# Kernel optimization log

Measured on AMD Instinct MI355X. Metric: run time of the kernel, lower is better.

The kernel has to match this reference:

```python
import jax, jax.numpy as jnp
import numpy as np

B, T, D, U, O = 256, 512, 256, 512, 64  # batch, n_steps, feature_in, units, n_output


def setup_inputs() -> dict:
    key = jax.random.key(0)
    k_x, k_wx, k_wh, k_wd = jax.random.split(key, 4)
    x = jax.random.normal(k_x, (B, T, D), dtype=jnp.float32)
    # Lecun-normal-ish init scales so activations stay sane
    Wx = jax.random.normal(k_wx, (D, 4 * U), dtype=jnp.float32) * (1.0 / np.sqrt(D))
    Wh = jax.random.normal(k_wh, (U, 4 * U), dtype=jnp.float32) * (1.0 / np.sqrt(U))
    b = jnp.zeros((4 * U,), dtype=jnp.float32)
    Wd = jax.random.normal(k_wd, (U, O), dtype=jnp.float32) * (1.0 / np.sqrt(U))
    bd = jnp.zeros((O,), dtype=jnp.float32)
    return {"x": x, "Wx": Wx, "Wh": Wh, "b": b, "Wd": Wd, "bd": bd}


def reference(x, Wx, Wh, b, Wd, bd):
    """Sequential LSTM scan (flax nn.LSTMCell math) + per-step dense decode.

    x: [B, T, D] -> y: [B, T, O]
    """
    batch = x.shape[0]
    units = Wh.shape[0]
    c0 = jnp.zeros((batch, units), dtype=x.dtype)
    h0 = jnp.zeros((batch, units), dtype=x.dtype)

    def step(carry, xt):
        c, h = carry
        gates = xt @ Wx + h @ Wh + b            # [B, 4U]
        i, f, g, o = jnp.split(gates, 4, axis=-1)
        i = jax.nn.sigmoid(i)
        f = jax.nn.sigmoid(f)
        g = jnp.tanh(g)
        o = jax.nn.sigmoid(o)
        c_new = f * c + i * g
        h_new = o * jnp.tanh(c_new)
        y = h_new @ Wd + bd                     # [B, O]
        return (c_new, h_new), y

    xs = jnp.swapaxes(x, 0, 1)                  # [T, B, D]
    _, ys = jax.lax.scan(step, (c0, h0), xs)    # ys: [T, B, O]
    return jnp.swapaxes(ys, 0, 1)               # [B, T, O]
```

## Files before the change

### kernel.cpp

```cpp
#include <hip/hip_runtime.h>


#define Bb 256
#define Tt 512
#define Dd 256
#define Uu 512
#define Oo 64

typedef short bs8 __attribute__((ext_vector_type(8)));
typedef float f32x4 __attribute__((ext_vector_type(4)));

__device__ __forceinline__ unsigned short f2bf(float f) {
  unsigned u = __float_as_uint(f);
  u += 0x7fffu + ((u >> 16) & 1u);
  return (unsigned short)(u >> 16);
}
__device__ __forceinline__ float bf2f(unsigned short s) {
  return __uint_as_float(((unsigned)s) << 16);
}
__device__ __forceinline__ float sigm(float v) { return 1.0f / (1.0f + __expf(-v)); }
__device__ __forceinline__ float tanhfast(float v) { return 2.0f / (1.0f + __expf(-2.0f * v)) - 1.0f; }

__device__ __forceinline__ int zbyte(int row, int k) {
  return (row * 1536 + k * 2) ^ ((row & 7) << 4);
}

__global__ void rnn_init_bar(unsigned* bar) {
  for (int i = threadIdx.x; i < 16 * 32 * 32; i += 256)
    __hip_atomic_store(&bar[i], 0u, __ATOMIC_RELAXED, __HIP_MEMORY_SCOPE_AGENT);
}

__launch_bounds__(256, 2)
__global__ void rnn_lstm_kernel(const float* __restrict__ x, const float* __restrict__ Wx,
                                const float* __restrict__ Wh, const float* __restrict__ bias,
                                const float* __restrict__ Wd, const float* __restrict__ bd,
                                float* __restrict__ out, unsigned short* hbuf, unsigned* bar) {
  __shared__ __align__(16) char zs[16 * 768 * 2];
  __shared__ float gates[4][16][17];
  __shared__ float wdl[512][2];
  __shared__ float ypart[16][2][16];

  const int tid = threadIdx.x;
  const int lane = tid & 63;
  const int wid = tid >> 6;
  const int bid = blockIdx.x;
  const int bg = (bid & 7) | ((bid >> 8) << 3);
  const int ug = (bid >> 3) & 31;
  const int b_base = bg * 16;
  const int u_base = ug * 16;
  const int oc0 = ug * 2;

  unsigned* fl = bar + bg * 32 * 32;

  bs8 breg[24];
  {
    const int gc = wid * 512 + u_base + (lane & 15);
    const int kfr = (lane >> 4) * 8;
#pragma unroll
    for (int ks = 0; ks < 24; ++ks) {
      bs8 bb;
#pragma unroll
      for (int e = 0; e < 8; ++e) {
        int kg = ks * 32 + kfr + e;
        float w = (kg < 256) ? Wx[(size_t)kg * 2048 + gc]
                             : Wh[(size_t)(kg - 256) * 2048 + gc];
        bb[e] = (short)f2bf(w);
      }
      breg[ks] = bb;
    }
  }

  const int prow = tid & 15;
  const int usec = tid >> 4;
  const int us4 = usec & 3;
  float bi[4], bff[4], bgg[4], boo[4];
  if (tid < 64) {
#pragma unroll
    for (int j = 0; j < 4; ++j) {
      int ugl = u_base + us4 * 4 + j;
      bi[j]  = bias[0 * 512 + ugl];
      bff[j] = bias[1 * 512 + ugl];
      bgg[j] = bias[2 * 512 + ugl];
      boo[j] = bias[3 * 512 + ugl];
    }
  }
  float cst[4] = {0.f, 0.f, 0.f, 0.f};

  union U16 { unsigned long long q[2]; bs8 v; };

#pragma unroll
  for (int i = 0; i < 4; ++i) {
    int c = tid + i * 256;
    int u = c >> 1, oc = c & 1;
    wdl[u][oc] = Wd[(size_t)u * Oo + oc0 + oc];
  }
  {
    int row = tid >> 4;
    int d0 = (tid & 15) * 16;
    const float* xp = x + ((size_t)(b_base + row) * Tt + 0) * Dd + d0;
    float4 v0 = *(const float4*)xp;
    float4 v1 = *(const float4*)(xp + 4);
    float4 v2 = *(const float4*)(xp + 8);
    float4 v3 = *(const float4*)(xp + 12);
    bs8 p0, p1;
    p0[0] = (short)f2bf(v0.x); p0[1] = (short)f2bf(v0.y);
    p0[2] = (short)f2bf(v0.z); p0[3] = (short)f2bf(v0.w);
    p0[4] = (short)f2bf(v1.x); p0[5] = (short)f2bf(v1.y);
    p0[6] = (short)f2bf(v1.z); p0[7] = (short)f2bf(v1.w);
    p1[0] = (short)f2bf(v2.x); p1[1] = (short)f2bf(v2.y);
    p1[2] = (short)f2bf(v2.z); p1[3] = (short)f2bf(v2.w);
    p1[4] = (short)f2bf(v3.x); p1[5] = (short)f2bf(v3.y);
    p1[6] = (short)f2bf(v3.z); p1[7] = (short)f2bf(v3.w);
    *(bs8*)(zs + zbyte(row, d0)) = p0;
    *(bs8*)(zs + zbyte(row, d0 + 8)) = p1;
  }
#pragma unroll
  for (int i = 0; i < 4; ++i) {
    int c = tid + i * 256;
    int row = c >> 6;
    int u0 = (c & 63) * 8;
    bs8 zz = {0, 0, 0, 0, 0, 0, 0, 0};
    *(bs8*)(zs + zbyte(row, 256 + u0)) = zz;
  }
  __syncthreads();

  for (int t = 0; t < Tt; ++t) {
    f32x4 acc0 = {0, 0, 0, 0}, acc1 = {0, 0, 0, 0};
    {
      const int arow = lane & 15;
      const int akf = (lane >> 4) * 8;
#pragma unroll
      for (int ks = 0; ks < 24; ks += 2) {
        bs8 av0 = *(const bs8*)(zs + zbyte(arow, ks * 32 + akf));
        bs8 av1 = *(const bs8*)(zs + zbyte(arow, (ks + 1) * 32 + akf));
        acc0 = __builtin_amdgcn_mfma_f32_16x16x32_bf16(av0, breg[ks], acc0, 0, 0, 0);
        acc1 = __builtin_amdgcn_mfma_f32_16x16x32_bf16(av1, breg[ks + 1], acc1, 0, 0, 0);
      }
      acc0 += acc1;
    }
    {
      const int u16 = lane & 15;
      const int rb = (lane >> 4) * 4;
#pragma unroll
      for (int j = 0; j < 4; ++j) gates[wid][rb + j][u16] = acc0[j];
    }
    __syncthreads();

    if (tid < 64) {
      unsigned long long hpack = 0ull;
#pragma unroll
      for (int j = 0; j < 4; ++j) {
        int u = us4 * 4 + j;
        float gi = gates[0][prow][u] + bi[j];
        float gf = gates[1][prow][u] + bff[j];
        float gg = gates[2][prow][u] + bgg[j];
        float go = gates[3][prow][u] + boo[j];
        float iv = sigm(gi), fv = sigm(gf), gv = tanhfast(gg), ov = sigm(go);
        float cn = fv * cst[j] + iv * gv;
        cst[j] = cn;
        float hv = ov * tanhfast(cn);
        hpack |= ((unsigned long long)f2bf(hv)) << (16 * j);
      }
      unsigned long long* hp =
          (unsigned long long*)(hbuf + (size_t)(t & 1) * Bb * Uu +
                                (size_t)(b_base + prow) * Uu + u_base + us4 * 4);
      unsigned long long old = __hip_atomic_exchange(hp, hpack, __ATOMIC_RELAXED,
                                                     __HIP_MEMORY_SCOPE_AGENT);
      asm volatile("" :: "v"(old));
    }
    __syncthreads();
    if (tid == 0) {
      unsigned oldf = __hip_atomic_exchange(&fl[ug * 32], (unsigned)(t + 1),
                                            __ATOMIC_RELAXED, __HIP_MEMORY_SCOPE_AGENT);
      asm volatile("" :: "v"(oldf));
    }

    if (t + 1 < Tt) {
      int row = tid >> 4;
      int d0 = (tid & 15) * 16;
      const float* xp = x + ((size_t)(b_base + row) * Tt + (t + 1)) * Dd + d0;
      float4 v0 = *(const float4*)xp;
      float4 v1 = *(const float4*)(xp + 4);
      float4 v2 = *(const float4*)(xp + 8);
      float4 v3 = *(const float4*)(xp + 12);
      bs8 p0, p1;
      p0[0] = (short)f2bf(v0.x); p0[1] = (short)f2bf(v0.y);
      p0[2] = (short)f2bf(v0.z); p0[3] = (short)f2bf(v0.w);
      p0[4] = (short)f2bf(v1.x); p0[5] = (short)f2bf(v1.y);
      p0[6] = (short)f2bf(v1.z); p0[7] = (short)f2bf(v1.w);
      p1[0] = (short)f2bf(v2.x); p1[1] = (short)f2bf(v2.y);
      p1[2] = (short)f2bf(v2.z); p1[3] = (short)f2bf(v2.w);
      p1[4] = (short)f2bf(v3.x); p1[5] = (short)f2bf(v3.y);
      p1[6] = (short)f2bf(v3.z); p1[7] = (short)f2bf(v3.w);
      *(bs8*)(zs + zbyte(row, d0)) = p0;
      *(bs8*)(zs + zbyte(row, d0 + 8)) = p1;
    }

    if (t > 0) {
      float s0 = 0.f, s1 = 0.f;
#pragma unroll
      for (int c8 = 0; c8 < 4; ++c8) {
        int k = 256 + usec * 32 + c8 * 8;
        bs8 hv = *(const bs8*)(zs + zbyte(prow, k));
#pragma unroll
        for (int e = 0; e < 8; ++e) {
          float hf = bf2f((unsigned short)hv[e]);
          int u = usec * 32 + c8 * 8 + e;
          s0 += hf * wdl[u][0];
          s1 += hf * wdl[u][1];
        }
      }
      ypart[prow][0][usec] = s0;
      ypart[prow][1][usec] = s1;
    }
    __syncthreads();
    if (t > 0 && tid < 32) {
      int b = tid >> 1, oc = tid & 1;
      float s = bd[oc0 + oc];
#pragma unroll
      for (int q = 0; q < 16; ++q) s += ypart[b][oc][q];
      out[((size_t)(b_base + b) * Tt + (t - 1)) * Oo + oc0 + oc] = s;
    }
    if (wid == 1) {
      for (;;) {
        unsigned v = __hip_atomic_load(&fl[(lane & 31) * 32], __ATOMIC_RELAXED,
                                       __HIP_MEMORY_SCOPE_AGENT);
        if (!__any((int)(v < (unsigned)(t + 1)))) break;
        __builtin_amdgcn_s_sleep(2);
      }
    }
    __builtin_amdgcn_sched_barrier(0);
    __syncthreads();

    {
      const unsigned short* hsrc = hbuf + (size_t)(t & 1) * Bb * Uu;
#pragma unroll
      for (int i = 0; i < 4; ++i) {
        int c = tid + i * 256;
        int row = c >> 6;
        int u0 = (c & 63) * 8;
        const unsigned long long* p =
            (const unsigned long long*)(hsrc + (size_t)(b_base + row) * Uu + u0);
        U16 uu;
        uu.q[0] = __hip_atomic_load(p, __ATOMIC_RELAXED, __HIP_MEMORY_SCOPE_AGENT);
        uu.q[1] = __hip_atomic_load(p + 1, __ATOMIC_RELAXED, __HIP_MEMORY_SCOPE_AGENT);
        *(bs8*)(zs + zbyte(row, 256 + u0)) = uu.v;
      }
    }
    __syncthreads();
  }

  {
    float s0 = 0.f, s1 = 0.f;
#pragma unroll
    for (int c8 = 0; c8 < 4; ++c8) {
      int k = 256 + usec * 32 + c8 * 8;
      bs8 hv = *(const bs8*)(zs + zbyte(prow, k));
#pragma unroll
      for (int e = 0; e < 8; ++e) {
        float hf = bf2f((unsigned short)hv[e]);
        int u = usec * 32 + c8 * 8 + e;
        s0 += hf * wdl[u][0];
        s1 += hf * wdl[u][1];
      }
    }
    ypart[prow][0][usec] = s0;
    ypart[prow][1][usec] = s1;
    __syncthreads();
    if (tid < 32) {
      int b = tid >> 1, oc = tid & 1;
      float s = bd[oc0 + oc];
#pragma unroll
      for (int q = 0; q < 16; ++q) s += ypart[b][oc][q];
      out[((size_t)(b_base + b) * Tt + (Tt - 1)) * Oo + oc0 + oc] = s;
    }
  }
}

extern "C" void kernel_launch(void* const* d_in, const int* in_sizes, int n_in,
                              void* d_out, int out_size, void* d_ws, size_t ws_size,
                              hipStream_t stream) {
  const float* x  = (const float*)d_in[0];
  const float* Wx = (const float*)d_in[1];
  const float* Wh = (const float*)d_in[2];
  const float* bs = (const float*)d_in[3];
  const float* Wd = (const float*)d_in[4];
  const float* bd = (const float*)d_in[5];
  float* out = (float*)d_out;

  unsigned short* hbuf = (unsigned short*)d_ws;
  unsigned* bar = (unsigned*)((char*)d_ws + (size_t)2 * Bb * Uu * 2);

  rnn_init_bar<<<1, 256, 0, stream>>>(bar);
  rnn_lstm_kernel<<<dim3(512), dim3(256), 0, stream>>>(x, Wx, Wh, bs, Wd, bd, out, hbuf, bar);
}
```

Measured before the change: 2.424 ms.

## Compute dense decode with MFMA and prefetch next-step x before gate matmul

The per-step output projection h@Wd, previously a scalar FMA loop over LDS-staged Wd with a 16-way partial reduction, now runs on MFMA with Wd held in registers as bf16 fragments (only 2 of 16 columns used). The decode is merged into the gate-matmul phase and its store into the cell-update phase, which removes one __syncthreads per step. The next timestep's x is loaded into registers before the matmul so global latency overlaps compute, and bf16 packing uses paired conversion intrinsics. Wd is now rounded to bf16, which lowers decode precision, and the extra fragment registers add pressure on top of 24 resident weight fragments.

```diff
diff --git a/kernel.cpp b/kernel.cpp
--- a/kernel.cpp
+++ b/kernel.cpp
@@ -1,4 +1,5 @@
 #include <hip/hip_runtime.h>
+#include <hip/hip_bf16.h>
 
 
 #define Bb 256
@@ -15,8 +16,10 @@
   u += 0x7fffu + ((u >> 16) & 1u);
   return (unsigned short)(u >> 16);
 }
-__device__ __forceinline__ float bf2f(unsigned short s) {
-  return __uint_as_float(((unsigned)s) << 16);
+__device__ __forceinline__ unsigned f2bf2(float lo, float hi) {
+  union { __hip_bfloat162 b; unsigned u; } cv;
+  cv.b = __float22bfloat162_rn(make_float2(lo, hi));
+  return cv.u;
 }
 __device__ __forceinline__ float sigm(float v) { return 1.0f / (1.0f + __expf(-v)); }
 __device__ __forceinline__ float tanhfast(float v) { return 2.0f / (1.0f + __expf(-2.0f * v)) - 1.0f; }
@@ -37,8 +40,7 @@
                                 float* __restrict__ out, unsigned short* hbuf, unsigned* bar) {
   __shared__ __align__(16) char zs[16 * 768 * 2];
   __shared__ float gates[4][16][17];
-  __shared__ float wdl[512][2];
-  __shared__ float ypart[16][2][16];
+  __shared__ float yp[4][16][2];
 
   const int tid = threadIdx.x;
   const int lane = tid & 63;
@@ -69,10 +71,25 @@
       breg[ks] = bb;
     }
   }
+  bs8 wdfrag[4];
+  {
+    const int col = lane & 15;
+    const int kfr = (lane >> 4) * 8;
+#pragma unroll
+    for (int i = 0; i < 4; ++i) {
+      int ksl = wid * 4 + i;
+      bs8 bb;
+#pragma unroll
+      for (int e = 0; e < 8; ++e) {
+        int u = ksl * 32 + kfr + e;
+        bb[e] = (col < 2) ? (short)f2bf(Wd[(size_t)u * Oo + oc0 + col]) : (short)0;
+      }
+      wdfrag[i] = bb;
+    }
+  }
 
   const int prow = tid & 15;
-  const int usec = tid >> 4;
-  const int us4 = usec & 3;
+  const int us4 = (tid >> 4) & 3;
   float bi[4], bff[4], bgg[4], boo[4];
   if (tid < 64) {
 #pragma unroll
@@ -88,12 +105,6 @@
 
   union U16 { unsigned long long q[2]; bs8 v; };
 
-#pragma unroll
-  for (int i = 0; i < 4; ++i) {
-    int c = tid + i * 256;
-    int u = c >> 1, oc = c & 1;
-    wdl[u][oc] = Wd[(size_t)u * Oo + oc0 + oc];
-  }
   {
     int row = tid >> 4;
     int d0 = (tid & 15) * 16;
@@ -102,17 +113,13 @@
     float4 v1 = *(const float4*)(xp + 4);
     float4 v2 = *(const float4*)(xp + 8);
     float4 v3 = *(const float4*)(xp + 12);
-    bs8 p0, p1;
-    p0[0] = (short)f2bf(v0.x); p0[1] = (short)f2bf(v0.y);
-    p0[2] = (short)f2bf(v0.z); p0[3] = (short)f2bf(v0.w);
-    p0[4] = (short)f2bf(v1.x); p0[5] = (short)f2bf(v1.y);
-    p0[6] = (short)f2bf(v1.z); p0[7] = (short)f2bf(v1.w);
-    p1[0] = (short)f2bf(v2.x); p1[1] = (short)f2bf(v2.y);
-    p1[2] = (short)f2bf(v2.z); p1[3] = (short)f2bf(v2.w);
-    p1[4] = (short)f2bf(v3.x); p1[5] = (short)f2bf(v3.y);
-    p1[6] = (short)f2bf(v3.z); p1[7] = (short)f2bf(v3.w);
-    *(bs8*)(zs + zbyte(row, d0)) = p0;
-    *(bs8*)(zs + zbyte(row, d0 + 8)) = p1;
+    uint4 p0, p1;
+    p0.x = f2bf2(v0.x, v0.y); p0.y = f2bf2(v0.z, v0.w);
+    p0.z = f2bf2(v1.x, v1.y); p0.w = f2bf2(v1.z, v1.w);
+    p1.x = f2bf2(v2.x, v2.y); p1.y = f2bf2(v2.z, v2.w);
+    p1.z = f2bf2(v3.x, v3.y); p1.w = f2bf2(v3.z, v3.w);
+    *(uint4*)(zs + zbyte(row, d0)) = p0;
+    *(uint4*)(zs + zbyte(row, d0 + 8)) = p1;
   }
 #pragma unroll
   for (int i = 0; i < 4; ++i) {
@@ -124,30 +131,53 @@
   }
   __syncthreads();
 
+  const int arow = lane & 15;
+  const int akf = (lane >> 4) * 8;
+  const int rb = (lane >> 4) * 4;
+
   for (int t = 0; t < Tt; ++t) {
+    float4 xv0, xv1, xv2, xv3;
+    const int xrow = tid >> 4;
+    const int xd0 = (tid & 15) * 16;
+    if (t + 1 < Tt) {
+      const float* xp = x + ((size_t)(b_base + xrow) * Tt + (t + 1)) * Dd + xd0;
+      xv0 = *(const float4*)xp;
+      xv1 = *(const float4*)(xp + 4);
+      xv2 = *(const float4*)(xp + 8);
+      xv3 = *(const float4*)(xp + 12);
+    }
+
     f32x4 acc0 = {0, 0, 0, 0}, acc1 = {0, 0, 0, 0};
+#pragma unroll
+    for (int ks = 0; ks < 24; ks += 2) {
+      bs8 av0 = *(const bs8*)(zs + zbyte(arow, ks * 32 + akf));
+      bs8 av1 = *(const bs8*)(zs + zbyte(arow, (ks + 1) * 32 + akf));
+      acc0 = __builtin_amdgcn_mfma_f32_16x16x32_bf16(av0, breg[ks], acc0, 0, 0, 0);
+      acc1 = __builtin_amdgcn_mfma_f32_16x16x32_bf16(av1, breg[ks + 1], acc1, 0, 0, 0);
+    }
+    acc0 += acc1;
     {
-      const int arow = lane & 15;
-      const int akf = (lane >> 4) * 8;
-#pragma unroll
-      for (int ks = 0; ks < 24; ks += 2) {
-        bs8 av0 = *(const bs8*)(zs + zbyte(arow, ks * 32 + akf));
-        bs8 av1 = *(const bs8*)(zs + zbyte(arow, (ks + 1) * 32 + akf));
-        acc0 = __builtin_amdgcn_mfma_f32_16x16x32_bf16(av0, breg[ks], acc0, 0, 0, 0);
-        acc1 = __builtin_amdgcn_mfma_f32_16x16x32_bf16(av1, breg[ks + 1], acc1, 0, 0, 0);
-      }
-      acc0 += acc1;
+      f32x4 yacc = {0, 0, 0, 0};
+#pragma unroll
+      for (int i = 0; i < 4; ++i) {
+        int ks = 8 + wid * 4 + i;
+        bs8 av = *(const bs8*)(zs + zbyte(arow, ks * 32 + akf));
+        yacc = __builtin_amdgcn_mfma_f32_16x16x32_bf16(av, wdfrag[i], yacc, 0, 0, 0);
+      }
+      if ((lane & 15) < 2) {
+#pragma unroll
+        for (int j = 0; j < 4; ++j) yp[wid][rb + j][lane & 15] = yacc[j];
+      }
     }
     {
       const int u16 = lane & 15;
-      const int rb = (lane >> 4) * 4;
 #pragma unroll
       for (int j = 0; j < 4; ++j) gates[wid][rb + j][u16] = acc0[j];
     }
     __syncthreads();
 
     if (tid < 64) {
-      unsigned long long hpack = 0ull;
+      float hv[4];
 #pragma unroll
       for (int j = 0; j < 4; ++j) {
         int u = us4 * 4 + j;
@@ -158,15 +188,21 @@
         float iv = sigm(gi), fv = sigm(gf), gv = tanhfast(gg), ov = sigm(go);
         float cn = fv * cst[j] + iv * gv;
         cst[j] = cn;
-        float hv = ov * tanhfast(cn);
-        hpack |= ((unsigned long long)f2bf(hv)) << (16 * j);
-      }
+        hv[j] = ov * tanhfast(cn);
+      }
+      unsigned long long hpack =
+          (unsigned long long)f2bf2(hv[0], hv[1]) |
+          ((unsigned long long)f2bf2(hv[2], hv[3]) << 32);
       unsigned long long* hp =
           (unsigned long long*)(hbuf + (size_t)(t & 1) * Bb * Uu +
                                 (size_t)(b_base + prow) * Uu + u_base + us4 * 4);
       unsigned long long old = __hip_atomic_exchange(hp, hpack, __ATOMIC_RELAXED,
                                                      __HIP_MEMORY_SCOPE_AGENT);
       asm volatile("" :: "v"(old));
+    } else if (t > 0 && tid >= 128 && tid < 160) {
+      int b = (tid - 128) >> 1, oc = tid & 1;
+      float s = bd[oc0 + oc] + yp[0][b][oc] + yp[1][b][oc] + yp[2][b][oc] + yp[3][b][oc];
+      out[((size_t)(b_base + b) * Tt + (t - 1)) * Oo + oc0 + oc] = s;
     }
     __syncthreads();
     if (tid == 0) {
@@ -176,50 +212,13 @@
     }
 
     if (t + 1 < Tt) {
-      int row = tid >> 4;
-      int d0 = (tid & 15) * 16;
-      const float* xp = x + ((size_t)(b_base + row) * Tt + (t + 1)) * Dd + d0;
-      float4 v0 = *(const float4*)xp;
-      float4 v1 = *(const float4*)(xp + 4);
-      float4 v2 = *(const float4*)(xp + 8);
-      float4 v3 = *(const float4*)(xp + 12);
-      bs8 p0, p1;
-      p0[0] = (short)f2bf(v0.x); p0[1] = (short)f2bf(v0.y);
-      p0[2] = (short)f2bf(v0.z); p0[3] = (short)f2bf(v0.w);
-      p0[4] = (short)f2bf(v1.x); p0[5] = (short)f2bf(v1.y);
-      p0[6] = (short)f2bf(v1.z); p0[7] = (short)f2bf(v1.w);
-      p1[0] = (short)f2bf(v2.x); p1[1] = (short)f2bf(v2.y);
-      p1[2] = (short)f2bf(v2.z); p1[3] = (short)f2bf(v2.w);
-      p1[4] = (short)f2bf(v3.x); p1[5] = (short)f2bf(v3.y);
-      p1[6] = (short)f2bf(v3.z); p1[7] = (short)f2bf(v3.w);
-      *(bs8*)(zs + zbyte(row, d0)) = p0;
-      *(bs8*)(zs + zbyte(row, d0 + 8)) = p1;
-    }
-
-    if (t > 0) {
-      float s0 = 0.f, s1 = 0.f;
-#pragma unroll
-      for (int c8 = 0; c8 < 4; ++c8) {
-        int k = 256 + usec * 32 + c8 * 8;
-        bs8 hv = *(const bs8*)(zs + zbyte(prow, k));
-#pragma unroll
-        for (int e = 0; e < 8; ++e) {
-          float hf = bf2f((unsigned short)hv[e]);
-          int u = usec * 32 + c8 * 8 + e;
-          s0 += hf * wdl[u][0];
-          s1 += hf * wdl[u][1];
-        }
-      }
-      ypart[prow][0][usec] = s0;
-      ypart[prow][1][usec] = s1;
-    }
-    __syncthreads();
-    if (t > 0 && tid < 32) {
-      int b = tid >> 1, oc = tid & 1;
-      float s = bd[oc0 + oc];
-#pragma unroll
-      for (int q = 0; q < 16; ++q) s += ypart[b][oc][q];
-      out[((size_t)(b_base + b) * Tt + (t - 1)) * Oo + oc0 + oc] = s;
+      uint4 p0, p1;
+      p0.x = f2bf2(xv0.x, xv0.y); p0.y = f2bf2(xv0.z, xv0.w);
+      p0.z = f2bf2(xv1.x, xv1.y); p0.w = f2bf2(xv1.z, xv1.w);
+      p1.x = f2bf2(xv2.x, xv2.y); p1.y = f2bf2(xv2.z, xv2.w);
+      p1.z = f2bf2(xv3.x, xv3.y); p1.w = f2bf2(xv3.z, xv3.w);
+      *(uint4*)(zs + zbyte(xrow, xd0)) = p0;
+      *(uint4*)(zs + zbyte(xrow, xd0 + 8)) = p1;
     }
     if (wid == 1) {
       for (;;) {
@@ -251,27 +250,21 @@
   }
 
   {
-    float s0 = 0.f, s1 = 0.f;
-#pragma unroll
-    for (int c8 = 0; c8 < 4; ++c8) {
-      int k = 256 + usec * 32 + c8 * 8;
-      bs8 hv = *(const bs8*)(zs + zbyte(prow, k));
-#pragma unroll
-      for (int e = 0; e < 8; ++e) {
-        float hf = bf2f((unsigned short)hv[e]);
-        int u = usec * 32 + c8 * 8 + e;
-        s0 += hf * wdl[u][0];
-        s1 += hf * wdl[u][1];
-      }
-    }
-    ypart[prow][0][usec] = s0;
-    ypart[prow][1][usec] = s1;
+    f32x4 yacc = {0, 0, 0, 0};
+#pragma unroll
+    for (int i = 0; i < 4; ++i) {
+      int ks = 8 + wid * 4 + i;
+      bs8 av = *(const bs8*)(zs + zbyte(arow, ks * 32 + akf));
+      yacc = __builtin_amdgcn_mfma_f32_16x16x32_bf16(av, wdfrag[i], yacc, 0, 0, 0);
+    }
+    if ((lane & 15) < 2) {
+#pragma unroll
+      for (int j = 0; j < 4; ++j) yp[wid][rb + j][lane & 15] = yacc[j];
+    }
     __syncthreads();
     if (tid < 32) {
       int b = tid >> 1, oc = tid & 1;
-      float s = bd[oc0 + oc];
-#pragma unroll
-      for (int q = 0; q < 16; ++q) s += ypart[b][oc][q];
+      float s = bd[oc0 + oc] + yp[0][b][oc] + yp[1][b][oc] + yp[2][b][oc] + yp[3][b][oc];
       out[((size_t)(b_base + b) * Tt + (Tt - 1)) * Oo + oc0 + oc] = s;
     }
   }
```

Measured after the change: 2.691 ms. 1.11x slower.

## Assign LSTM work by XCD so each batch group's barrier stays within one XCD

Applied to the files above, without the earlier changes.

Each block reads its hardware XCC id and takes a slot from a per-XCD atomic counter. The slot determines its batch group and unit group, so all 32 blocks sharing a batch-group barrier run on the same XCD. Flag publish and polling then switch to workgroup-scope atomics (polling becomes a fetch_add of zero), aiming to keep barrier traffic in the XCD-local L2 instead of going cross-die. Extra dynamic LDS is requested, which changes occupancy. This relies on blocks being spread evenly across XCDs and on weaker-scope atomics still being visible to other CUs, which risks incorrect synchronisation or deadlock.

```diff
diff --git a/kernel.cpp b/kernel.cpp
--- a/kernel.cpp
+++ b/kernel.cpp
@@ -26,7 +26,7 @@
 }
 
 __global__ void rnn_init_bar(unsigned* bar) {
-  for (int i = threadIdx.x; i < 16 * 32 * 32; i += 256)
+  for (int i = threadIdx.x; i < 16 * 32 * 32 + 8 * 32; i += 256)
     __hip_atomic_store(&bar[i], 0u, __ATOMIC_RELAXED, __HIP_MEMORY_SCOPE_AGENT);
 }
 
@@ -39,13 +39,24 @@
   __shared__ float gates[4][16][17];
   __shared__ float wdl[512][2];
   __shared__ float ypart[16][2][16];
+  __shared__ unsigned slotsh;
 
   const int tid = threadIdx.x;
   const int lane = tid & 63;
   const int wid = tid >> 6;
-  const int bid = blockIdx.x;
-  const int bg = (bid & 7) | ((bid >> 8) << 3);
-  const int ug = (bid >> 3) & 31;
+
+  unsigned xcd;
+  asm("s_getreg_b32 %0, hwreg(HW_REG_XCC_ID)" : "=s"(xcd));
+  xcd &= 7u;
+  if (tid == 0) {
+    unsigned* cnts = bar + 16 * 32 * 32;
+    slotsh = __hip_atomic_fetch_add(&cnts[xcd * 32], 1u, __ATOMIC_RELAXED,
+                                    __HIP_MEMORY_SCOPE_AGENT);
+  }
+  __syncthreads();
+  const unsigned s = slotsh & 63u;
+  const int bg = (int)xcd + 8 * (int)(s & 1u);
+  const int ug = (int)(s >> 1) & 31;
   const int b_base = bg * 16;
   const int u_base = ug * 16;
   const int oc0 = ug * 2;
@@ -171,7 +182,7 @@
     __syncthreads();
     if (tid == 0) {
       unsigned oldf = __hip_atomic_exchange(&fl[ug * 32], (unsigned)(t + 1),
-                                            __ATOMIC_RELAXED, __HIP_MEMORY_SCOPE_AGENT);
+                                            __ATOMIC_RELAXED, __HIP_MEMORY_SCOPE_WORKGROUP);
       asm volatile("" :: "v"(oldf));
     }
 
@@ -216,15 +227,17 @@
     __syncthreads();
     if (t > 0 && tid < 32) {
       int b = tid >> 1, oc = tid & 1;
-      float s = bd[oc0 + oc];
-#pragma unroll
-      for (int q = 0; q < 16; ++q) s += ypart[b][oc][q];
-      out[((size_t)(b_base + b) * Tt + (t - 1)) * Oo + oc0 + oc] = s;
+      float s2 = bd[oc0 + oc];
+#pragma unroll
+      for (int q = 0; q < 16; ++q) s2 += ypart[b][oc][q];
+      out[((size_t)(b_base + b) * Tt + (t - 1)) * Oo + oc0 + oc] = s2;
     }
     if (wid == 1) {
+      unsigned zero = 0;
+      asm volatile("" : "+v"(zero));
       for (;;) {
-        unsigned v = __hip_atomic_load(&fl[(lane & 31) * 32], __ATOMIC_RELAXED,
-                                       __HIP_MEMORY_SCOPE_AGENT);
+        unsigned v = __hip_atomic_fetch_add(&fl[(lane & 31) * 32], zero,
+                                            __ATOMIC_RELAXED, __HIP_MEMORY_SCOPE_WORKGROUP);
         if (!__any((int)(v < (unsigned)(t + 1)))) break;
         __builtin_amdgcn_s_sleep(2);
       }
@@ -269,10 +282,10 @@
     __syncthreads();
     if (tid < 32) {
       int b = tid >> 1, oc = tid & 1;
-      float s = bd[oc0 + oc];
-#pragma unroll
-      for (int q = 0; q < 16; ++q) s += ypart[b][oc][q];
-      out[((size_t)(b_base + b) * Tt + (Tt - 1)) * Oo + oc0 + oc] = s;
+      float s2 = bd[oc0 + oc];
+#pragma unroll
+      for (int q = 0; q < 16; ++q) s2 += ypart[b][oc][q];
+      out[((size_t)(b_base + b) * Tt + (Tt - 1)) * Oo + oc0 + oc] = s2;
     }
   }
 }
@@ -292,5 +305,6 @@
   unsigned* bar = (unsigned*)((char*)d_ws + (size_t)2 * Bb * Uu * 2);
 
   rnn_init_bar<<<1, 256, 0, stream>>>(bar);
-  rnn_lstm_kernel<<<dim3(512), dim3(256), 0, stream>>>(x, Wx, Wh, bs, Wd, bd, out, hbuf, bar);
-}
+  rnn_lstm_kernel<<<dim3(512), dim3(256), 24576, stream>>>(x, Wx, Wh, bs, Wd, bd,
+                                                           out, hbuf, bar);
+}
```

Measured after the change: 2.949 ms. 21.7% more time.

## Process 32 batch rows per block and halve the persistent grid to 256 blocks

Applied to the files above, without the earlier changes.

Each block now covers 32 batch rows instead of 16, issuing two MFMA row tiles per wave that reuse the same register-resident weight fragments. The grid shrinks from 512 to 256 blocks with one block per CU, so fewer blocks take part in each cross-block flag barrier. The aim is to cut per-step sync and weight-reuse overhead at the price of more per-block work and LDS use on the serial critical path.

```diff
diff --git a/kernel.cpp b/kernel.cpp
--- a/kernel.cpp
+++ b/kernel.cpp
@@ -26,27 +26,27 @@
 }
 
 __global__ void rnn_init_bar(unsigned* bar) {
-  for (int i = threadIdx.x; i < 16 * 32 * 32; i += 256)
+  for (int i = threadIdx.x; i < 8 * 32 * 32; i += 256)
     __hip_atomic_store(&bar[i], 0u, __ATOMIC_RELAXED, __HIP_MEMORY_SCOPE_AGENT);
 }
 
-__launch_bounds__(256, 2)
+__launch_bounds__(256, 1)
 __global__ void rnn_lstm_kernel(const float* __restrict__ x, const float* __restrict__ Wx,
                                 const float* __restrict__ Wh, const float* __restrict__ bias,
                                 const float* __restrict__ Wd, const float* __restrict__ bd,
                                 float* __restrict__ out, unsigned short* hbuf, unsigned* bar) {
-  __shared__ __align__(16) char zs[16 * 768 * 2];
-  __shared__ float gates[4][16][17];
+  __shared__ __align__(16) char zs[32 * 768 * 2];
+  __shared__ float gates[4][32][17];
   __shared__ float wdl[512][2];
-  __shared__ float ypart[16][2][16];
+  __shared__ float ypart[32][2][8];
 
   const int tid = threadIdx.x;
   const int lane = tid & 63;
   const int wid = tid >> 6;
   const int bid = blockIdx.x;
-  const int bg = (bid & 7) | ((bid >> 8) << 3);
-  const int ug = (bid >> 3) & 31;
-  const int b_base = bg * 16;
+  const int bg = bid & 7;
+  const int ug = bid >> 3;
+  const int b_base = bg * 32;
   const int u_base = ug * 16;
   const int oc0 = ug * 2;
 
@@ -70,11 +70,11 @@
     }
   }
 
-  const int prow = tid & 15;
-  const int usec = tid >> 4;
-  const int us4 = usec & 3;
+  const int prow = tid & 31;
+  const int sec = tid >> 5;
+  const int us4 = sec & 3;
   float bi[4], bff[4], bgg[4], boo[4];
-  if (tid < 64) {
+  if (tid < 128) {
 #pragma unroll
     for (int j = 0; j < 4; ++j) {
       int ugl = u_base + us4 * 4 + j;
@@ -91,31 +91,26 @@
 #pragma unroll
   for (int i = 0; i < 4; ++i) {
     int c = tid + i * 256;
-    int u = c >> 1, oc = c & 1;
-    wdl[u][oc] = Wd[(size_t)u * Oo + oc0 + oc];
+    wdl[c >> 1][c & 1] = Wd[(size_t)(c >> 1) * Oo + oc0 + (c & 1)];
   }
   {
-    int row = tid >> 4;
-    int d0 = (tid & 15) * 16;
+    int row = tid >> 3;
+    int d0 = (tid & 7) * 32;
     const float* xp = x + ((size_t)(b_base + row) * Tt + 0) * Dd + d0;
-    float4 v0 = *(const float4*)xp;
-    float4 v1 = *(const float4*)(xp + 4);
-    float4 v2 = *(const float4*)(xp + 8);
-    float4 v3 = *(const float4*)(xp + 12);
-    bs8 p0, p1;
-    p0[0] = (short)f2bf(v0.x); p0[1] = (short)f2bf(v0.y);
-    p0[2] = (short)f2bf(v0.z); p0[3] = (short)f2bf(v0.w);
-    p0[4] = (short)f2bf(v1.x); p0[5] = (short)f2bf(v1.y);
-    p0[6] = (short)f2bf(v1.z); p0[7] = (short)f2bf(v1.w);
-    p1[0] = (short)f2bf(v2.x); p1[1] = (short)f2bf(v2.y);
-    p1[2] = (short)f2bf(v2.z); p1[3] = (short)f2bf(v2.w);
-    p1[4] = (short)f2bf(v3.x); p1[5] = (short)f2bf(v3.y);
-    p1[6] = (short)f2bf(v3.z); p1[7] = (short)f2bf(v3.w);
-    *(bs8*)(zs + zbyte(row, d0)) = p0;
-    *(bs8*)(zs + zbyte(row, d0 + 8)) = p1;
-  }
-#pragma unroll
-  for (int i = 0; i < 4; ++i) {
+#pragma unroll
+    for (int q = 0; q < 4; ++q) {
+      float4 va = *(const float4*)(xp + q * 8);
+      float4 vb = *(const float4*)(xp + q * 8 + 4);
+      bs8 pk;
+      pk[0] = (short)f2bf(va.x); pk[1] = (short)f2bf(va.y);
+      pk[2] = (short)f2bf(va.z); pk[3] = (short)f2bf(va.w);
+      pk[4] = (short)f2bf(vb.x); pk[5] = (short)f2bf(vb.y);
+      pk[6] = (short)f2bf(vb.z); pk[7] = (short)f2bf(vb.w);
+      *(bs8*)(zs + zbyte(row, d0 + q * 8)) = pk;
+    }
+  }
+#pragma unroll
+  for (int i = 0; i < 8; ++i) {
     int c = tid + i * 256;
     int row = c >> 6;
     int u0 = (c & 63) * 8;
@@ -124,29 +119,33 @@
   }
   __syncthreads();
 
+  const int arow = lane & 15;
+  const int akf = (lane >> 4) * 8;
+  const int rb = (lane >> 4) * 4;
+  const int u16 = lane & 15;
+
   for (int t = 0; t < Tt; ++t) {
-    f32x4 acc0 = {0, 0, 0, 0}, acc1 = {0, 0, 0, 0};
-    {
-      const int arow = lane & 15;
-      const int akf = (lane >> 4) * 8;
-#pragma unroll
-      for (int ks = 0; ks < 24; ks += 2) {
-        bs8 av0 = *(const bs8*)(zs + zbyte(arow, ks * 32 + akf));
-        bs8 av1 = *(const bs8*)(zs + zbyte(arow, (ks + 1) * 32 + akf));
-        acc0 = __builtin_amdgcn_mfma_f32_16x16x32_bf16(av0, breg[ks], acc0, 0, 0, 0);
-        acc1 = __builtin_amdgcn_mfma_f32_16x16x32_bf16(av1, breg[ks + 1], acc1, 0, 0, 0);
-      }
-      acc0 += acc1;
-    }
-    {
-      const int u16 = lane & 15;
-      const int rb = (lane >> 4) * 4;
-#pragma unroll
-      for (int j = 0; j < 4; ++j) gates[wid][rb + j][u16] = acc0[j];
-    }
-    __syncthreads();
-
-    if (tid < 64) {
+    f32x4 aA0 = {0,0,0,0}, aA1 = {0,0,0,0}, aB0 = {0,0,0,0}, aB1 = {0,0,0,0};
+#pragma unroll
+    for (int ks = 0; ks < 24; ks += 2) {
+      bs8 a00 = *(const bs8*)(zs + zbyte(arow,      ks * 32 + akf));
+      bs8 a01 = *(const bs8*)(zs + zbyte(arow,      (ks + 1) * 32 + akf));
+      bs8 a10 = *(const bs8*)(zs + zbyte(arow + 16, ks * 32 + akf));
+      bs8 a11 = *(const bs8*)(zs + zbyte(arow + 16, (ks + 1) * 32 + akf));
+      aA0 = __builtin_amdgcn_mfma_f32_16x16x32_bf16(a00, breg[ks], aA0, 0, 0, 0);
+      aA1 = __builtin_amdgcn_mfma_f32_16x16x32_bf16(a01, breg[ks + 1], aA1, 0, 0, 0);
+      aB0 = __builtin_amdgcn_mfma_f32_16x16x32_bf16(a10, breg[ks], aB0, 0, 0, 0);
+      aB1 = __builtin_amdgcn_mfma_f32_16x16x32_bf16(a11, breg[ks + 1], aB1, 0, 0, 0);
+    }
+    aA0 += aA1; aB0 += aB1;
+#pragma unroll
+    for (int j = 0; j < 4; ++j) {
+      gates[wid][rb + j][u16]      = aA0[j];
+      gates[wid][16 + rb + j][u16] = aB0[j];
+    }
+    __syncthreads();
+
+    if (tid < 128) {
       unsigned long long hpack = 0ull;
 #pragma unroll
       for (int j = 0; j < 4; ++j) {
@@ -176,49 +175,45 @@
     }
 
     if (t + 1 < Tt) {
-      int row = tid >> 4;
-      int d0 = (tid & 15) * 16;
+      int row = tid >> 3;
+      int d0 = (tid & 7) * 32;
       const float* xp = x + ((size_t)(b_base + row) * Tt + (t + 1)) * Dd + d0;
-      float4 v0 = *(const float4*)xp;
-      float4 v1 = *(const float4*)(xp + 4);
-      float4 v2 = *(const float4*)(xp + 8);
-      float4 v3 = *(const float4*)(xp + 12);
-      bs8 p0, p1;
-      p0[0] = (short)f2bf(v0.x); p0[1] = (short)f2bf(v0.y);
-      p0[2] = (short)f2bf(v0.z); p0[3] = (short)f2bf(v0.w);
-      p0[4] = (short)f2bf(v1.x); p0[5] = (short)f2bf(v1.y);
-      p0[6] = (short)f2bf(v1.z); p0[7] = (short)f2bf(v1.w);
-      p1[0] = (short)f2bf(v2.x); p1[1] = (short)f2bf(v2.y);
-      p1[2] = (short)f2bf(v2.z); p1[3] = (short)f2bf(v2.w);
-      p1[4] = (short)f2bf(v3.x); p1[5] = (short)f2bf(v3.y);
-      p1[6] = (short)f2bf(v3.z); p1[7] = (short)f2bf(v3.w);
-      *(bs8*)(zs + zbyte(row, d0)) = p0;
-      *(bs8*)(zs + zbyte(row, d0 + 8)) = p1;
+#pragma unroll
+      for (int q = 0; q < 4; ++q) {
+        float4 va = *(const float4*)(xp + q * 8);
+        float4 vb = *(const float4*)(xp + q * 8 + 4);
+        bs8 pk;
+        pk[0] = (short)f2bf(va.x); pk[1] = (short)f2bf(va.y);
+        pk[2] = (short)f2bf(va.z); pk[3] = (short)f2bf(va.w);
+        pk[4] = (short)f2bf(vb.x); pk[5] = (short)f2bf(vb.y);
+        pk[6] = (short)f2bf(vb.z); pk[7] = (short)f2bf(vb.w);
+        *(bs8*)(zs + zbyte(row, d0 + q * 8)) = pk;
+      }
     }
 
     if (t > 0) {
       float s0 = 0.f, s1 = 0.f;
 #pragma unroll
-      for (int c8 = 0; c8 < 4; ++c8) {
-        int k = 256 + usec * 32 + c8 * 8;
+      for (int c8 = 0; c8 < 8; ++c8) {
+        int k = 256 + sec * 64 + c8 * 8;
         bs8 hv = *(const bs8*)(zs + zbyte(prow, k));
 #pragma unroll
         for (int e = 0; e < 8; ++e) {
           float hf = bf2f((unsigned short)hv[e]);
-          int u = usec * 32 + c8 * 8 + e;
+          int u = sec * 64 + c8 * 8 + e;
           s0 += hf * wdl[u][0];
           s1 += hf * wdl[u][1];
         }
       }
-      ypart[prow][0][usec] = s0;
-      ypart[prow][1][usec] = s1;
-    }
-    __syncthreads();
-    if (t > 0 && tid < 32) {
+      ypart[prow][0][sec] = s0;
+      ypart[prow][1][sec] = s1;
+    }
+    __syncthreads();
+    if (t > 0 && tid < 64) {
       int b = tid >> 1, oc = tid & 1;
       float s = bd[oc0 + oc];
 #pragma unroll
-      for (int q = 0; q < 16; ++q) s += ypart[b][oc][q];
+      for (int q = 0; q < 8; ++q) s += ypart[b][oc][q];
       out[((size_t)(b_base + b) * Tt + (t - 1)) * Oo + oc0 + oc] = s;
     }
     if (wid == 1) {
@@ -235,7 +230,7 @@
     {
       const unsigned short* hsrc = hbuf + (size_t)(t & 1) * Bb * Uu;
 #pragma unroll
-      for (int i = 0; i < 4; ++i) {
+      for (int i = 0; i < 8; ++i) {
         int c = tid + i * 256;
         int row = c >> 6;
         int u0 = (c & 63) * 8;
@@ -253,27 +248,27 @@
   {
     float s0 = 0.f, s1 = 0.f;
 #pragma unroll
-    for (int c8 = 0; c8 < 4; ++c8) {
-      int k = 256 + usec * 32 + c8 * 8;
+    for (int c8 = 0; c8 < 8; ++c8) {
+      int k = 256 + sec * 64 + c8 * 8;
       bs8 hv = *(const bs8*)(zs + zbyte(prow, k));
 #pragma unroll
       for (int e = 0; e < 8; ++e) {
         float hf = bf2f((unsigned short)hv[e]);
-        int u = usec * 32 + c8 * 8 + e;
+        int u = sec * 64 + c8 * 8 + e;
         s0 += hf * wdl[u][0];
         s1 += hf * wdl[u][1];
       }
     }
-    ypart[prow][0][usec] = s0;
-    ypart[prow][1][usec] = s1;
-    __syncthreads();
-    if (tid < 32) {
-      int b = tid >> 1, oc = tid & 1;
-      float s = bd[oc0 + oc];
-#pragma unroll
-      for (int q = 0; q < 16; ++q) s += ypart[b][oc][q];
-      out[((size_t)(b_base + b) * Tt + (Tt - 1)) * Oo + oc0 + oc] = s;
-    }
+    ypart[prow][0][sec] = s0;
+    ypart[prow][1][sec] = s1;
+  }
+  __syncthreads();
+  if (tid < 64) {
+    int b = tid >> 1, oc = tid & 1;
+    float s = bd[oc0 + oc];
+#pragma unroll
+    for (int q = 0; q < 8; ++q) s += ypart[b][oc][q];
+    out[((size_t)(b_base + b) * Tt + (Tt - 1)) * Oo + oc0 + oc] = s;
   }
 }
 
@@ -292,5 +287,5 @@
   unsigned* bar = (unsigned*)((char*)d_ws + (size_t)2 * Bb * Uu * 2);
 
   rnn_init_bar<<<1, 256, 0, stream>>>(bar);
-  rnn_lstm_kernel<<<dim3(512), dim3(256), 0, stream>>>(x, Wx, Wh, bs, Wd, bd, out, hbuf, bar);
-}
+  rnn_lstm_kernel<<<dim3(256), dim3(256), 0, stream>>>(x, Wx, Wh, bs, Wd, bd, out, hbuf, bar);
+}
```

New measurement: 3.668 ms. 1.51x slower.
